# Optimization experiments

Hardware: AMD Instinct MI355X
Metric: run time of the kernel (lower is better)

The kernel has to match this reference:

```python
import jax, jax.numpy as jnp
import numpy as np

NEG_SLOPE = 0.2  # PyG GATConv default leaky_relu slope


def gat_conv(x, src, dst, n, W, a_src, a_dst, b):
    """Single-head PyG GATConv (self-loops already included in src/dst)."""
    h = x @ W                                  # [N, F]
    alpha_s = h @ a_src                        # [N]
    alpha_d = h @ a_dst                        # [N]
    e = jax.nn.leaky_relu(alpha_s[src] + alpha_d[dst], NEG_SLOPE)  # [E]
    m = jax.ops.segment_max(e, dst, num_segments=n)
    e = jnp.exp(e - m[dst])
    s = jax.ops.segment_sum(e, dst, num_segments=n)
    alpha = e / s[dst]                         # softmax over incoming edges
    out = jax.ops.segment_sum(alpha[:, None] * h[src], dst, num_segments=n)
    return out + b


def setup_inputs() -> dict:
    key = jax.random.key(0)
    ks = jax.random.split(key, 12)
    N, E = 8192, 262144
    IN, H, OUT, K = 512, 128, 64, 16
    x = jax.random.normal(ks[0], (N, IN), dtype=jnp.float32)
    edge_index = jax.random.randint(ks[1], (2, E), 0, N, dtype=jnp.int32)
    def glorot(k, shape):
        lim = np.sqrt(6.0 / (shape[0] + shape[-1]))
        return jax.random.uniform(k, shape, jnp.float32, -lim, lim)
    return {
        "x": x,
        "edge_index": edge_index,
        "W1": glorot(ks[2], (IN, H)),
        "a_src1": glorot(ks[3], (H,)),
        "a_dst1": glorot(ks[4], (H,)),
        "b1": jnp.zeros((H,), jnp.float32),
        "W2": glorot(ks[5], (H, OUT)),
        "a_src2": glorot(ks[6], (OUT,)),
        "a_dst2": glorot(ks[7], (OUT,)),
        "b2": jnp.zeros((OUT,), jnp.float32),
        "centers": glorot(ks[8], (K, OUT)),
    }


def reference(x, edge_index, W1, a_src1, a_dst1, b1, W2, a_src2, a_dst2, b2, centers):
    n = x.shape[0]
    # add self loops (PyG GATConv default add_self_loops=True)
    loop = jnp.arange(n, dtype=edge_index.dtype)
    src = jnp.concatenate([edge_index[0], loop])
    dst = jnp.concatenate([edge_index[1], loop])
    h = jax.nn.elu(gat_conv(x, src, dst, n, W1, a_src1, a_dst1, b1))
    z = gat_conv(h, src, dst, n, W2, a_src2, a_dst2, b2)       # [N, D]
    A_pred = jax.nn.sigmoid(z @ z.T)                            # [N, N]
    # Student-t soft assignment: [N, K]
    d2 = jnp.sum((z[:, None, :] - centers[None, :, :]) ** 2, axis=2)
    q = 1.0 / (1.0 + d2)
    q = q / jnp.sum(q, axis=1, keepdims=True)
    return (z, A_pred, q)
```

## Files before the change

### kernel.cpp

```cpp
#include <hip/hip_runtime.h>
#include <hip/hip_bf16.h>

typedef __bf16 v8bf __attribute__((ext_vector_type(8)));
typedef unsigned short v8us __attribute__((ext_vector_type(8)));
typedef float  v4f  __attribute__((ext_vector_type(4)));

__device__ __forceinline__ float lrelu02(float x){ return x > 0.f ? x : 0.2f*x; }

__device__ __forceinline__ unsigned short f2bf_rn(float f){
  unsigned int u = __float_as_uint(f);
  u += 0x7fffu + ((u >> 16) & 1u);
  return (unsigned short)(u >> 16);
}
__device__ __forceinline__ float bf2f(unsigned short h){
  return __uint_as_float(((unsigned int)h) << 16);
}

union BF8cast { v8us u; v8bf b; };

__global__ void hist_kernel(const int* __restrict__ dst, int* counts, int E){
  int i = blockIdx.x*blockDim.x + threadIdx.x;
  if (i < E) atomicAdd(&counts[dst[i]], 1);
}

__global__ void scan_kernel(const int* __restrict__ counts, int* ptr, int* cursor, int n){
  __shared__ int sd[1024];
  int t = threadIdx.x;
  int base = t*8;
  int v[8]; int s = 0;
  #pragma unroll
  for (int i = 0; i < 8; ++i){ int x = (base+i < n) ? counts[base+i] : 0; v[i] = x; s += x; }
  sd[t] = s; __syncthreads();
  for (int off = 1; off < 1024; off <<= 1){
    int x = (t >= off) ? sd[t-off] : 0;
    __syncthreads();
    sd[t] += x;
    __syncthreads();
  }
  int run = sd[t] - s;
  #pragma unroll
  for (int i = 0; i < 8; ++i){
    if (base+i < n){ ptr[base+i] = run; cursor[base+i] = run; run += v[i]; }
  }
  if (t == 1023) ptr[n] = run;
}

__global__ void scatter_kernel(const int* __restrict__ src, const int* __restrict__ dst,
                               int* cursor, int* csr_src, int E){
  int i = blockIdx.x*blockDim.x + threadIdx.x;
  if (i < E){
    int p = atomicAdd(&cursor[dst[i]], 1);
    csr_src[p] = src[i];
  }
}

__global__ void prep_kernel(const float* __restrict__ W1,
    unsigned short* wth, unsigned short* wtl, int* counts, int nw, int n){
  int i = blockIdx.x*blockDim.x + threadIdx.x;
  if (i < nw){
    int k = i >> 7, c = i & 127;
    float f = W1[i];
    unsigned short h = f2bf_rn(f);
    wth[c*512 + k] = h;
    wtl[c*512 + k] = f2bf_rn(f - bf2f(h));
  } else if (i < nw + n){
    counts[i - nw] = 0;
  }
}

__global__ __launch_bounds__(128) void gemm1_fused(const float* __restrict__ x,
    const unsigned short* __restrict__ wth, const unsigned short* __restrict__ wtl,
    const float* __restrict__ avs, const float* __restrict__ avd,
    float* __restrict__ h1, float* __restrict__ as_out, float* __restrict__ ad_out){
  const int lane = threadIdx.x & 63;
  const int wave = threadIdx.x >> 6;
  const int i0 = blockIdx.x*32 + wave*16;
  const int r = lane & 15, q = lane >> 4;
  const float* xr = x + (size_t)(i0 + r)*512;
  v4f acc[8];
  #pragma unroll
  for (int c = 0; c < 8; ++c) acc[c] = (v4f){0.f,0.f,0.f,0.f};
  for (int kt = 0; kt < 16; ++kt){
    int k = kt*32 + q*8;
    v4f xa = *reinterpret_cast<const v4f*>(xr + k);
    v4f xb = *reinterpret_cast<const v4f*>(xr + k + 4);
    v8us ahu, alu;
    #pragma unroll
    for (int j = 0; j < 8; ++j){
      float f = (j < 4) ? xa[j] : xb[j-4];
      unsigned short hh = f2bf_rn(f);
      ahu[j] = hh;
      alu[j] = f2bf_rn(f - bf2f(hh));
    }
    BF8cast ch; ch.u = ahu;
    BF8cast cl; cl.u = alu;
    v8bf ah = ch.b, al = cl.b;
    #pragma unroll
    for (int ct = 0; ct < 8; ++ct){
      v8bf bh = *reinterpret_cast<const v8bf*>(wth + (size_t)(ct*16 + r)*512 + k);
      v8bf bl = *reinterpret_cast<const v8bf*>(wtl + (size_t)(ct*16 + r)*512 + k);
      acc[ct] = __builtin_amdgcn_mfma_f32_16x16x32_bf16(ah, bh, acc[ct], 0,0,0);
      acc[ct] = __builtin_amdgcn_mfma_f32_16x16x32_bf16(al, bh, acc[ct], 0,0,0);
      acc[ct] = __builtin_amdgcn_mfma_f32_16x16x32_bf16(ah, bl, acc[ct], 0,0,0);
    }
  }
  #pragma unroll
  for (int ct = 0; ct < 8; ++ct)
    #pragma unroll
    for (int t = 0; t < 4; ++t)
      h1[(size_t)(i0 + q*4 + t)*128 + ct*16 + r] = acc[ct][t];
  float sa[4] = {0.f,0.f,0.f,0.f}, da[4] = {0.f,0.f,0.f,0.f};
  #pragma unroll
  for (int ct = 0; ct < 8; ++ct){
    float ws = avs[ct*16 + r], wd = avd[ct*16 + r];
    #pragma unroll
    for (int t = 0; t < 4; ++t){ sa[t] += acc[ct][t]*ws; da[t] += acc[ct][t]*wd; }
  }
  #pragma unroll
  for (int off = 1; off < 16; off <<= 1){
    #pragma unroll
    for (int t = 0; t < 4; ++t){
      sa[t] += __shfl_xor(sa[t], off);
      da[t] += __shfl_xor(da[t], off);
    }
  }
  if (r == 0){
    #pragma unroll
    for (int t = 0; t < 4; ++t){
      as_out[i0 + q*4 + t] = sa[t];
      ad_out[i0 + q*4 + t] = da[t];
    }
  }
}

__global__ void gat_agg1(const float* __restrict__ h, const float* __restrict__ as,
                         const float* __restrict__ ad, const int* __restrict__ ptr,
                         const int* __restrict__ csr_src, const float* __restrict__ bias,
                         float* __restrict__ out, int n){
  const int F = 128;
  int wid = (blockIdx.x*blockDim.x + threadIdx.x) >> 6;
  int lane = threadIdx.x & 63;
  if (wid >= n) return;
  const int v = wid;
  const int beg = ptr[v], end = ptr[v+1];
  const int deg = end - beg;
  const float adv = ad[v];
  const float asv = as[v];
  const float eself = lrelu02(asv + adv);
  int sv0 = v; float e0 = -3.4e38f;
  if (lane < deg){ sv0 = csr_src[beg + lane]; e0 = lrelu02(as[sv0] + adv); }
  float m = fmaxf(eself, e0);
  for (int j = beg + 64 + lane; j < end; j += 64)
    m = fmaxf(m, lrelu02(as[csr_src[j]] + adv));
  for (int o = 32; o; o >>= 1) m = fmaxf(m, __shfl_xor(m, o));
  float wv0 = (lane < deg) ? __expf(e0 - m) : 0.f;
  float wself = __expf(eself - m);
  float ssum = wv0 + ((lane == 0) ? wself : 0.f);
  const int half = lane >> 5, l32 = lane & 31;
  v4f acc = (v4f){0.f,0.f,0.f,0.f};
  if (half == 0){
    v4f hv = *reinterpret_cast<const v4f*>(h + (size_t)v*F + l32*4);
    acc += hv * wself;
  }
  {
    int cnt = min(64, deg);
    for (int t = 0; t < cnt; t += 2){
      int idx = t + half;
      float wt = __shfl(wv0, idx);
      int   st = __shfl(sv0, idx);
      if (idx >= cnt){ wt = 0.f; st = v; }
      v4f hv = *reinterpret_cast<const v4f*>(h + (size_t)st*F + l32*4);
      acc += hv * wt;
    }
  }
  for (int b0 = beg + 64; b0 < end; b0 += 64){
    int j = b0 + lane;
    float wv = 0.f; int sv = v;
    if (j < end){
      sv = csr_src[j];
      wv = __expf(lrelu02(as[sv] + adv) - m);
      ssum += wv;
    }
    int cnt = min(64, end - b0);
    for (int t = 0; t < cnt; t += 2){
      int idx = t + half;
      float wt = __shfl(wv, idx);
      int   st = __shfl(sv, idx);
      if (idx >= cnt){ wt = 0.f; st = v; }
      v4f hv = *reinterpret_cast<const v4f*>(h + (size_t)st*F + l32*4);
      acc += hv * wt;
    }
  }
  for (int o = 32; o; o >>= 1) ssum += __shfl_xor(ssum, o);
  #pragma unroll
  for (int c = 0; c < 4; ++c) acc[c] += __shfl_xor(acc[c], 32);
  if (half == 0){
    float inv = 1.f / ssum;
    v4f bv = *reinterpret_cast<const v4f*>(bias + l32*4);
    v4f rr;
    #pragma unroll
    for (int c = 0; c < 4; ++c){
      float r0 = acc[c]*inv + bv[c];
      rr[c] = r0 > 0.f ? r0 : __expf(r0) - 1.f;
    }
    *reinterpret_cast<v4f*>(out + (size_t)v*F + l32*4) = rr;
  }
}

template<int BM,int BN,int BK,int TM,int TN>
__global__ __launch_bounds__(256) void gemm2_fused(const float* __restrict__ A,
    const float* __restrict__ B, float* __restrict__ C, int M, int N, int K,
    const float* __restrict__ avs, const float* __restrict__ avd,
    float* __restrict__ as_out, float* __restrict__ ad_out){
  __shared__ float As[BK][BM+1];
  __shared__ float Bs[BK][BN+1];
  __shared__ float reds[BM][17];
  __shared__ float redd[BM][17];
  const int tid = threadIdx.x;
  const int tx = tid % (BN/TN);
  const int ty = tid / (BN/TN);
  const int brow = blockIdx.y*BM;
  const int bcol = blockIdx.x*BN;
  float acc[TM][TN] = {};
  for (int k0 = 0; k0 < K; k0 += BK){
    for (int i = tid; i < BM*BK; i += 256){
      int m = i / BK, kk = i % BK;
      As[kk][m] = A[(size_t)(brow+m)*K + k0 + kk];
    }
    for (int i = tid; i < BK*BN; i += 256){
      int kk = i / BN, nn = i % BN;
      Bs[kk][nn] = B[(size_t)(k0+kk)*N + bcol + nn];
    }
    __syncthreads();
    #pragma unroll
    for (int kk = 0; kk < BK; ++kk){
      float a[TM], b[TN];
      #pragma unroll
      for (int m = 0; m < TM; ++m) a[m] = As[kk][ty*TM+m];
      #pragma unroll
      for (int n = 0; n < TN; ++n) b[n] = Bs[kk][tx*TN+n];
      #pragma unroll
      for (int m = 0; m < TM; ++m)
        #pragma unroll
        for (int n = 0; n < TN; ++n) acc[m][n] += a[m]*b[n];
    }
    __syncthreads();
  }
  float ps[TM] = {}, pd[TM] = {};
  #pragma unroll
  for (int m = 0; m < TM; ++m){
    #pragma unroll
    for (int n = 0; n < TN; ++n){
      float c = acc[m][n];
      C[(size_t)(brow+ty*TM+m)*N + bcol+tx*TN+n] = c;
      float s = avs[bcol+tx*TN+n], d = avd[bcol+tx*TN+n];
      ps[m] += c*s; pd[m] += c*d;
    }
  }
  #pragma unroll
  for (int m = 0; m < TM; ++m){
    reds[ty*TM+m][tx] = ps[m];
    redd[ty*TM+m][tx] = pd[m];
  }
  __syncthreads();
  if (tid < BM){
    float s = 0.f, d = 0.f;
    #pragma unroll
    for (int k = 0; k < BN/TN; ++k){ s += reds[tid][k]; d += redd[tid][k]; }
    as_out[brow + tid] = s;
    ad_out[brow + tid] = d;
  }
}

__global__ void gat_agg2_fused(const float* __restrict__ h, const float* __restrict__ as,
                               const float* __restrict__ ad, const int* __restrict__ ptr,
                               const int* __restrict__ csr_src, const float* __restrict__ bias,
                               const float* __restrict__ centers,
                               float* __restrict__ z_out, unsigned short* __restrict__ zhi,
                               unsigned short* __restrict__ zlo, float* __restrict__ qout,
                               int n, int K){
  const int F = 64;
  int wid = (blockIdx.x*blockDim.x + threadIdx.x) >> 6;
  int lane = threadIdx.x & 63;
  if (wid >= n) return;
  const int v = wid;
  const int beg = ptr[v], end = ptr[v+1];
  const int deg = end - beg;
  const float adv = ad[v];
  const float asv = as[v];
  const float eself = lrelu02(asv + adv);
  int sv0 = v; float e0 = -3.4e38f;
  if (lane < deg){ sv0 = csr_src[beg + lane]; e0 = lrelu02(as[sv0] + adv); }
  float m = fmaxf(eself, e0);
  for (int j = beg + 64 + lane; j < end; j += 64)
    m = fmaxf(m, lrelu02(as[csr_src[j]] + adv));
  for (int o = 32; o; o >>= 1) m = fmaxf(m, __shfl_xor(m, o));
  float wv0 = (lane < deg) ? __expf(e0 - m) : 0.f;
  float wself = __expf(eself - m);
  float ssum = wv0 + ((lane == 0) ? wself : 0.f);
  const int qr = lane >> 4, l16 = lane & 15;
  v4f acc = (v4f){0.f,0.f,0.f,0.f};
  if (qr == 0){
    v4f hv = *reinterpret_cast<const v4f*>(h + (size_t)v*F + l16*4);
    acc += hv * wself;
  }
  {
    int cnt = min(64, deg);
    for (int t = 0; t < cnt; t += 4){
      int idx = t + qr;
      float wt = __shfl(wv0, idx);
      int   st = __shfl(sv0, idx);
      if (idx >= cnt){ wt = 0.f; st = v; }
      v4f hv = *reinterpret_cast<const v4f*>(h + (size_t)st*F + l16*4);
      acc += hv * wt;
    }
  }
  for (int b0 = beg + 64; b0 < end; b0 += 64){
    int j = b0 + lane;
    float wv = 0.f; int sv = v;
    if (j < end){
      sv = csr_src[j];
      wv = __expf(lrelu02(as[sv] + adv) - m);
      ssum += wv;
    }
    int cnt = min(64, end - b0);
    for (int t = 0; t < cnt; t += 4){
      int idx = t + qr;
      float wt = __shfl(wv, idx);
      int   st = __shfl(sv, idx);
      if (idx >= cnt){ wt = 0.f; st = v; }
      v4f hv = *reinterpret_cast<const v4f*>(h + (size_t)st*F + l16*4);
      acc += hv * wt;
    }
  }
  for (int o = 32; o; o >>= 1) ssum += __shfl_xor(ssum, o);
  #pragma unroll
  for (int c = 0; c < 4; ++c){
    acc[c] += __shfl_xor(acc[c], 16);
    acc[c] += __shfl_xor(acc[c], 32);
  }
  int srcLane = lane >> 2;
  float c0 = __shfl(acc[0], srcLane);
  float c1 = __shfl(acc[1], srcLane);
  float c2 = __shfl(acc[2], srcLane);
  float c3 = __shfl(acc[3], srcLane);
  int sel = lane & 3;
  float av = sel == 0 ? c0 : sel == 1 ? c1 : sel == 2 ? c2 : c3;
  float r0 = av / ssum + bias[lane];
  z_out[(size_t)v*F + lane] = r0;
  unsigned short hh = f2bf_rn(r0);
  zhi[(size_t)v*F + lane] = hh;
  zlo[(size_t)v*F + lane] = f2bf_rn(r0 - bf2f(hh));
  float myq = 0.f, tot = 0.f;
  for (int k = 0; k < K; ++k){
    float d = r0 - centers[k*F + lane];
    float d2 = d*d;
    for (int o = 32; o; o >>= 1) d2 += __shfl_xor(d2, o);
    float qq = 1.f / (1.f + d2);
    if (lane == k) myq = qq;
    tot += qq;
  }
  if (lane < K) qout[(size_t)v*K + lane] = myq / tot;
}

__device__ __forceinline__ v8bf ldz(const unsigned short* z, int node, int k){
  return *reinterpret_cast<const v8bf*>(z + ((size_t)node << 6) + k);
}

__global__ __launch_bounds__(256) void apred_kernel(const unsigned short* __restrict__ zhi,
    const unsigned short* __restrict__ zlo, float* __restrict__ out, int N){
  __shared__ float tile[4][16][132];
  const int nwg = gridDim.x * gridDim.y;
  int wg = blockIdx.y * gridDim.x + blockIdx.x;
  int cpx = nwg >> 3;
  int swz = (wg & 7) * cpx + (wg >> 3);
  int by = swz / gridDim.x;
  int bx = swz - by * gridDim.x;
  const int lane = threadIdx.x & 63;
  const int wave = threadIdx.x >> 6;
  const int i0 = by*64 + wave*16;
  const int j0 = bx*128;
  const int r = lane & 15, q = lane >> 4;
  const int arow = i0 + r;
  v8bf ahi0 = ldz(zhi, arow,      q*8);
  v8bf ahi1 = ldz(zhi, arow, 32 + q*8);
  v8bf alo0 = ldz(zlo, arow,      q*8);
  v8bf alo1 = ldz(zlo, arow, 32 + q*8);
  #pragma unroll
  for (int c = 0; c < 8; ++c){
    int brow = j0 + c*16 + r;
    v8bf bhi0 = ldz(zhi, brow,      q*8);
    v8bf bhi1 = ldz(zhi, brow, 32 + q*8);
    v8bf blo0 = ldz(zlo, brow,      q*8);
    v8bf blo1 = ldz(zlo, brow, 32 + q*8);
    v4f acc = {0.f,0.f,0.f,0.f};
    acc = __builtin_amdgcn_mfma_f32_16x16x32_bf16(ahi0, bhi0, acc, 0,0,0);
    acc = __builtin_amdgcn_mfma_f32_16x16x32_bf16(ahi1, bhi1, acc, 0,0,0);
    acc = __builtin_amdgcn_mfma_f32_16x16x32_bf16(ahi0, blo0, acc, 0,0,0);
    acc = __builtin_amdgcn_mfma_f32_16x16x32_bf16(ahi1, blo1, acc, 0,0,0);
    acc = __builtin_amdgcn_mfma_f32_16x16x32_bf16(alo0, bhi0, acc, 0,0,0);
    acc = __builtin_amdgcn_mfma_f32_16x16x32_bf16(alo1, bhi1, acc, 0,0,0);
    #pragma unroll
    for (int t = 0; t < 4; ++t){
      float e = __expf(-acc[t]);
      tile[wave][q*4 + t][c*16 + r] = __builtin_amdgcn_rcpf(1.f + e);
    }
  }
  #pragma unroll
  for (int t = 0; t < 8; ++t){
    int row = t*2 + (lane >> 5);
    int col = (lane & 31)*4;
    v4f vv = *reinterpret_cast<v4f*>(&tile[wave][row][col]);
    __builtin_nontemporal_store(vv, reinterpret_cast<v4f*>(out + (size_t)(i0 + row)*N + j0 + col));
  }
}

extern "C" void kernel_launch(void* const* d_in, const int* in_sizes, int n_in,
                              void* d_out, int out_size, void* d_ws, size_t ws_size,
                              hipStream_t stream) {
  const float* x      = (const float*)d_in[0];
  const int*   ei     = (const int*)  d_in[1];
  const float* W1     = (const float*)d_in[2];
  const float* a_src1 = (const float*)d_in[3];
  const float* a_dst1 = (const float*)d_in[4];
  const float* b1     = (const float*)d_in[5];
  const float* W2     = (const float*)d_in[6];
  const float* a_src2 = (const float*)d_in[7];
  const float* a_dst2 = (const float*)d_in[8];
  const float* b2     = (const float*)d_in[9];
  const float* cent   = (const float*)d_in[10];

  const int H   = in_sizes[3];
  const int OUTF= in_sizes[7];
  const int INF = in_sizes[2] / H;
  const int N   = in_sizes[0] / INF;
  const int E   = in_sizes[1] / 2;
  const int K   = in_sizes[10] / OUTF;

  const int* e_src = ei;
  const int* e_dst = ei + E;

  char* wsp = (char*)d_ws;
  auto alloc = [&](size_t b)->void*{ void* p = (void*)wsp; wsp += (b + 255) & ~(size_t)255; return p; };
  int* counts   = (int*)alloc((size_t)N*4);
  int* ptr      = (int*)alloc((size_t)(N+1)*4);
  int* cursor   = (int*)alloc((size_t)N*4);
  int* csr_src  = (int*)alloc((size_t)E*4);
  float* as1    = (float*)alloc((size_t)N*4);
  float* ad1    = (float*)alloc((size_t)N*4);
  float* as2    = (float*)alloc((size_t)N*4);
  float* ad2    = (float*)alloc((size_t)N*4);
  unsigned short* zhi = (unsigned short*)alloc((size_t)N*OUTF*2);
  unsigned short* zlo = (unsigned short*)alloc((size_t)N*OUTF*2);
  unsigned short* wth = (unsigned short*)alloc((size_t)INF*H*2);
  unsigned short* wtl = (unsigned short*)alloc((size_t)INF*H*2);

  float* out_f  = (float*)d_out;
  float* z_out  = out_f;
  float* ap_out = out_f + (size_t)N*OUTF;
  float* q_out  = ap_out + (size_t)N*N;
  float* h1  = ap_out;
  float* h2  = h1 + (size_t)N*H;
  float* h2w = h2 + (size_t)N*H;

  const int wavesPerGrid = (N*64 + 255)/256;
  const int nw = INF*H;

  prep_kernel<<<(nw + N + 255)/256, 256, 0, stream>>>(W1, wth, wtl, counts, nw, N);
  hist_kernel<<<(E+255)/256, 256, 0, stream>>>(e_dst, counts, E);
  scan_kernel<<<1, 1024, 0, stream>>>(counts, ptr, cursor, N);
  scatter_kernel<<<(E+255)/256, 256, 0, stream>>>(e_src, e_dst, cursor, csr_src, E);
  gemm1_fused<<<N/32, 128, 0, stream>>>(x, wth, wtl, a_src1, a_dst1, h1, as1, ad1);
  gat_agg1<<<wavesPerGrid, 256, 0, stream>>>(h1, as1, ad1, ptr, csr_src, b1, h2, N);
  gemm2_fused<64,64,16,4,4><<<dim3(OUTF/64, N/64), 256, 0, stream>>>(h2, W2, h2w, N, OUTF, H,
                                                                     a_src2, a_dst2, as2, ad2);
  gat_agg2_fused<<<wavesPerGrid, 256, 0, stream>>>(h2w, as2, ad2, ptr, csr_src, b2, cent,
                                                   z_out, zhi, zlo, q_out, N, K);
  apred_kernel<<<dim3(N/128, N/64), 256, 0, stream>>>(zhi, zlo, ap_out, N);
}
```

Measured before the change: 528.2 us.

## Fuse second-layer GEMM and attention projections into first aggregation kernel

```diff
diff --git a/kernel.cpp b/kernel.cpp
--- a/kernel.cpp
+++ b/kernel.cpp
@@ -136,7 +136,10 @@
 __global__ void gat_agg1(const float* __restrict__ h, const float* __restrict__ as,
                          const float* __restrict__ ad, const int* __restrict__ ptr,
                          const int* __restrict__ csr_src, const float* __restrict__ bias,
-                         float* __restrict__ out, int n){
+                         const float* __restrict__ W2, const float* __restrict__ avs2,
+                         const float* __restrict__ avd2,
+                         float* __restrict__ h2w, float* __restrict__ as2,
+                         float* __restrict__ ad2, int n){
   const int F = 128;
   int wid = (blockIdx.x*blockDim.x + threadIdx.x) >> 6;
   int lane = threadIdx.x & 63;
@@ -194,82 +197,25 @@
   for (int o = 32; o; o >>= 1) ssum += __shfl_xor(ssum, o);
   #pragma unroll
   for (int c = 0; c < 4; ++c) acc[c] += __shfl_xor(acc[c], 32);
-  if (half == 0){
-    float inv = 1.f / ssum;
-    v4f bv = *reinterpret_cast<const v4f*>(bias + l32*4);
-    v4f rr;
-    #pragma unroll
-    for (int c = 0; c < 4; ++c){
-      float r0 = acc[c]*inv + bv[c];
-      rr[c] = r0 > 0.f ? r0 : __expf(r0) - 1.f;
-    }
-    *reinterpret_cast<v4f*>(out + (size_t)v*F + l32*4) = rr;
-  }
-}
-
-template<int BM,int BN,int BK,int TM,int TN>
-__global__ __launch_bounds__(256) void gemm2_fused(const float* __restrict__ A,
-    const float* __restrict__ B, float* __restrict__ C, int M, int N, int K,
-    const float* __restrict__ avs, const float* __restrict__ avd,
-    float* __restrict__ as_out, float* __restrict__ ad_out){
-  __shared__ float As[BK][BM+1];
-  __shared__ float Bs[BK][BN+1];
-  __shared__ float reds[BM][17];
-  __shared__ float redd[BM][17];
-  const int tid = threadIdx.x;
-  const int tx = tid % (BN/TN);
-  const int ty = tid / (BN/TN);
-  const int brow = blockIdx.y*BM;
-  const int bcol = blockIdx.x*BN;
-  float acc[TM][TN] = {};
-  for (int k0 = 0; k0 < K; k0 += BK){
-    for (int i = tid; i < BM*BK; i += 256){
-      int m = i / BK, kk = i % BK;
-      As[kk][m] = A[(size_t)(brow+m)*K + k0 + kk];
-    }
-    for (int i = tid; i < BK*BN; i += 256){
-      int kk = i / BN, nn = i % BN;
-      Bs[kk][nn] = B[(size_t)(k0+kk)*N + bcol + nn];
-    }
-    __syncthreads();
-    #pragma unroll
-    for (int kk = 0; kk < BK; ++kk){
-      float a[TM], b[TN];
-      #pragma unroll
-      for (int m = 0; m < TM; ++m) a[m] = As[kk][ty*TM+m];
-      #pragma unroll
-      for (int n = 0; n < TN; ++n) b[n] = Bs[kk][tx*TN+n];
-      #pragma unroll
-      for (int m = 0; m < TM; ++m)
-        #pragma unroll
-        for (int n = 0; n < TN; ++n) acc[m][n] += a[m]*b[n];
-    }
-    __syncthreads();
-  }
-  float ps[TM] = {}, pd[TM] = {};
-  #pragma unroll
-  for (int m = 0; m < TM; ++m){
-    #pragma unroll
-    for (int n = 0; n < TN; ++n){
-      float c = acc[m][n];
-      C[(size_t)(brow+ty*TM+m)*N + bcol+tx*TN+n] = c;
-      float s = avs[bcol+tx*TN+n], d = avd[bcol+tx*TN+n];
-      ps[m] += c*s; pd[m] += c*d;
-    }
-  }
-  #pragma unroll
-  for (int m = 0; m < TM; ++m){
-    reds[ty*TM+m][tx] = ps[m];
-    redd[ty*TM+m][tx] = pd[m];
-  }
-  __syncthreads();
-  if (tid < BM){
-    float s = 0.f, d = 0.f;
-    #pragma unroll
-    for (int k = 0; k < BN/TN; ++k){ s += reds[tid][k]; d += redd[tid][k]; }
-    as_out[brow + tid] = s;
-    ad_out[brow + tid] = d;
-  }
+  float inv = 1.f / ssum;
+  v4f bv = *reinterpret_cast<const v4f*>(bias + l32*4);
+  v4f rr;
+  #pragma unroll
+  for (int c = 0; c < 4; ++c){
+    float r0 = acc[c]*inv + bv[c];
+    rr[c] = r0 > 0.f ? r0 : __expf(r0) - 1.f;
+  }
+  float hw = 0.f;
+  #pragma unroll
+  for (int k = 0; k < 128; ++k){
+    float rk = __shfl(rr[k & 3], k >> 2);
+    hw += rk * W2[(size_t)k*64 + lane];
+  }
+  h2w[(size_t)v*64 + lane] = hw;
+  float ps = hw * avs2[lane];
+  float pd = hw * avd2[lane];
+  for (int o = 32; o; o >>= 1){ ps += __shfl_xor(ps, o); pd += __shfl_xor(pd, o); }
+  if (lane == 0){ as2[v] = ps; ad2[v] = pd; }
 }
 
 __global__ void gat_agg2_fused(const float* __restrict__ h, const float* __restrict__ as,
@@ -460,8 +406,7 @@
   float* ap_out = out_f + (size_t)N*OUTF;
   float* q_out  = ap_out + (size_t)N*N;
   float* h1  = ap_out;
-  float* h2  = h1 + (size_t)N*H;
-  float* h2w = h2 + (size_t)N*H;
+  float* h2w = h1 + (size_t)N*H;
 
   const int wavesPerGrid = (N*64 + 255)/256;
   const int nw = INF*H;
@@ -471,9 +416,8 @@
   scan_kernel<<<1, 1024, 0, stream>>>(counts, ptr, cursor, N);
   scatter_kernel<<<(E+255)/256, 256, 0, stream>>>(e_src, e_dst, cursor, csr_src, E);
   gemm1_fused<<<N/32, 128, 0, stream>>>(x, wth, wtl, a_src1, a_dst1, h1, as1, ad1);
-  gat_agg1<<<wavesPerGrid, 256, 0, stream>>>(h1, as1, ad1, ptr, csr_src, b1, h2, N);
-  gemm2_fused<64,64,16,4,4><<<dim3(OUTF/64, N/64), 256, 0, stream>>>(h2, W2, h2w, N, OUTF, H,
-                                                                     a_src2, a_dst2, as2, ad2);
+  gat_agg1<<<wavesPerGrid, 256, 0, stream>>>(h1, as1, ad1, ptr, csr_src, b1,
+                                             W2, a_src2, a_dst2, h2w, as2, ad2, N);
   gat_agg2_fused<<<wavesPerGrid, 256, 0, stream>>>(h2w, as2, ad2, ptr, csr_src, b2, cent,
                                                    z_out, zhi, zlo, q_out, N, K);
   apred_kernel<<<dim3(N/128, N/64), 256, 0, stream>>>(zhi, zlo, ap_out, N);
```

New measurement: 514.9 us. -2.5%, faster.
